# Optimization experiments

Hardware: AMD Instinct MI355X
Metric: run time of the kernel (lower is better)

## Reference

```python
import jax, jax.numpy as jnp
import numpy as np

B, N, D, H = 16, 1024, 768, 12
HD = D // H
SCALE = HD ** -0.5


def setup_inputs() -> dict:
    key = jax.random.key(0)
    ks = jax.random.split(key, 7)
    s = D ** -0.5
    return {
        "x": jax.random.normal(ks[0], (B, N, D), dtype=jnp.float32),
        "Wq": jax.random.normal(ks[1], (D, D), dtype=jnp.float32) * s,
        "bq": jax.random.normal(ks[2], (D,), dtype=jnp.float32) * 0.01,
        "Wk": jax.random.normal(ks[3], (D, D), dtype=jnp.float32) * s,
        "bk": jax.random.normal(ks[4], (D,), dtype=jnp.float32) * 0.01,
        "Wv": jax.random.normal(ks[5], (D, D), dtype=jnp.float32) * s,
        "bv": jax.random.normal(ks[6], (D,), dtype=jnp.float32) * 0.01,
    }


def _split_heads(t):
    # [B, N, D] -> [B, H, N, HD]
    return t.reshape(B, N, H, HD).transpose(0, 2, 1, 3)


def reference(x, Wq, bq, Wk, bk, Wv, bv):
    q = _split_heads(x @ Wq + bq)
    k = _split_heads(x @ Wk + bk)
    v = _split_heads(x @ Wv + bv)
    # [B, H, N, N] attention scores, fp32 softmax (matches eager path)
    scores = jnp.einsum("bhqd,bhkd->bhqk", q, k) * SCALE
    attn = jax.nn.softmax(scores.astype(jnp.float32), axis=-1).astype(q.dtype)
    # dropout p=0 in eval mode -> identity
    ctx = jnp.einsum("bhqk,bhkd->bhqd", attn, v)  # [B, H, N, HD]
    ctx = ctx.transpose(0, 2, 1, 3).reshape(B, N, D)
    return ctx
```

## Files before the change

### kernel.cpp

```cpp
#include <hip/hip_runtime.h>

#define B_ 16
#define N_ 1024
#define D_ 768
#define H_ 12
#define HD_ 64
#define QSCALE 0.18033688011112042f

typedef __attribute__((ext_vector_type(8))) __bf16 bf16x8;
typedef __attribute__((ext_vector_type(4))) float f32x4;
typedef unsigned short u16;
typedef unsigned int u32;

__device__ inline u16 f2bf(float f) {
    u32 u = __builtin_bit_cast(u32, f);
    u += 0x7fffu + ((u >> 16) & 1u);
    return (u16)(u >> 16);
}

__device__ inline float fexp2(float x) {
#if __has_builtin(__builtin_amdgcn_exp2f)
    return __builtin_amdgcn_exp2f(x);
#else
    return exp2f(x);
#endif
}

__device__ inline u32 cvt_pk_bf16(float a, float b) {
    u32 r;
    asm("v_cvt_pk_bf16_f32 %0, %1, %2" : "=v"(r) : "v"(a), "v"(b));
    return r;
}

__device__ inline void gl_lds16(const u16* gp, u16* lp_) {
    __builtin_amdgcn_global_load_lds(
        (const __attribute__((address_space(1))) u32*)(gp),
        (__attribute__((address_space(3))) u32*)(lp_), 16, 0, 0);
}

__global__ __launch_bounds__(256) void prep_kernel(
    const float* __restrict__ x, u16* __restrict__ xbf,
    const float* __restrict__ Wq, const float* __restrict__ Wk,
    const float* __restrict__ Wv, u16* __restrict__ wtall) {
    const int bid = blockIdx.x, tid = threadIdx.x;
    if (bid < 6144) {
        int i = bid * 256 + tid;
        const float4* p = (const float4*)x;
        float4 a = p[2 * i], b = p[2 * i + 1];
        union { u16 us[8]; int4 v; } u;
        u.us[0] = f2bf(a.x); u.us[1] = f2bf(a.y); u.us[2] = f2bf(a.z); u.us[3] = f2bf(a.w);
        u.us[4] = f2bf(b.x); u.us[5] = f2bf(b.y); u.us[6] = f2bf(b.z); u.us[7] = f2bf(b.w);
        ((int4*)xbf)[i] = u.v;
    } else {
        __shared__ u16 t[32][33];
        int wb = bid - 6144;
        int z = wb / 576, rem = wb % 576;
        int bx = rem % 24, by = rem / 24;
        const float* W = z == 0 ? Wq : (z == 1 ? Wk : Wv);
        u16* Wt = wtall + (size_t)z * D_ * D_;
        int n0 = bx * 32, k0 = by * 32;
        int tx = tid & 31, ty = tid >> 5;
#pragma unroll
        for (int i = 0; i < 4; i++) {
            int k = k0 + ty + i * 8;
            t[ty + i * 8][tx] = f2bf(W[k * D_ + n0 + tx]);
        }
        __syncthreads();
#pragma unroll
        for (int i = 0; i < 4; i++) {
            int n = n0 + ty + i * 8;
            Wt[n * D_ + k0 + tx] = t[tx][ty + i * 8];
        }
    }
}

__global__ __launch_bounds__(512, 2) void qkv2_kernel(
    const u16* __restrict__ xbf, const u16* __restrict__ wtall,
    const float* __restrict__ bq, const float* __restrict__ bk, const float* __restrict__ bv,
    u16* __restrict__ qbf, u16* __restrict__ kbf, u16* __restrict__ vtbf) {
    __shared__ u16 lsA[4 * 8192];
    __shared__ u16 lsB[4 * 8192];

    const int mt = blockIdx.x, nt = blockIdx.y;
    const int tid = threadIdx.x, w = tid >> 6, lane = tid & 63;
    const int g = lane >> 4, c = lane & 15;
    const int wm = w >> 2, wn = w & 3;
    const int m0 = mt * 256, n0 = nt * 192;

    const int srow = w * 16 + (lane >> 2);
    const int gch = (lane & 3) ^ ((lane >> 3) & 3);
    const u16* sa0 = xbf + (size_t)(m0 + srow) * D_ + gch * 8;
    const u16* sa1 = xbf + (size_t)(m0 + 128 + srow) * D_ + gch * 8;
    const u16* sb0 = wtall + (size_t)(n0 + srow) * D_ + gch * 8;
    const u16* sb1 = wtall + (size_t)(n0 + 128 + srow) * D_ + gch * 8;

#define STAGEP(slot, p) do {                                          \
        gl_lds16(sa0 + (p) * 32, &lsA[(slot) * 8192 + w * 512]);        \
        gl_lds16(sa1 + (p) * 32, &lsA[(slot) * 8192 + 4096 + w * 512]); \
        gl_lds16(sb0 + (p) * 32, &lsB[(slot) * 8192 + w * 512]);        \
        gl_lds16(sb1 + (p) * 32, &lsB[(slot) * 8192 + 4096 + w * 512]); \
    } while (0)

    f32x4 acc[8][3];
#pragma unroll
    for (int i = 0; i < 8; i++)
#pragma unroll
        for (int j = 0; j < 3; j++) acc[i][j] = (f32x4){0.f, 0.f, 0.f, 0.f};

    const int gp8 = (g ^ ((c >> 1) & 3)) * 8;

#define COMPUTE(s) do {                                                         \
        bf16x8 af[8], bfr[3];                                                   \
        _Pragma("unroll")                                                       \
        for (int fr = 0; fr < 8; fr++)                                          \
            af[fr] = *(const bf16x8*)&lsA[(s) * 8192 + (wm * 128 + fr * 16 + c) * 32 + gp8]; \
        _Pragma("unroll")                                                       \
        for (int fc = 0; fc < 3; fc++)                                          \
            bfr[fc] = *(const bf16x8*)&lsB[(s) * 8192 + (wn * 48 + fc * 16 + c) * 32 + gp8]; \
        _Pragma("unroll")                                                       \
        for (int fr = 0; fr < 8; fr++)                                          \
            _Pragma("unroll")                                                   \
            for (int fc = 0; fc < 3; fc++)                                      \
                acc[fr][fc] = __builtin_amdgcn_mfma_f32_16x16x32_bf16(          \
                    af[fr], bfr[fc], acc[fr][fc], 0, 0, 0);                     \
    } while (0)

    STAGEP(0, 0);
    STAGEP(1, 1);
    for (int p = 0; p < 22; ++p) {
        STAGEP((p + 2) & 3, p + 2);
        asm volatile("s_waitcnt vmcnt(8)" ::: "memory");
        __builtin_amdgcn_s_barrier();
        __builtin_amdgcn_sched_barrier(0);
        COMPUTE(p & 3);
    }
    asm volatile("s_waitcnt vmcnt(4)" ::: "memory");
    __builtin_amdgcn_s_barrier();
    __builtin_amdgcn_sched_barrier(0);
    COMPUTE(2);
    asm volatile("s_waitcnt vmcnt(0)" ::: "memory");
    __builtin_amdgcn_s_barrier();
    __builtin_amdgcn_sched_barrier(0);
    COMPUTE(3);
#undef STAGEP
#undef COMPUTE

    const int mode = nt >> 2;
    const int msub = nt & 3;
    const float* bias = mode == 0 ? bq : (mode == 1 ? bk : bv);
    float bb[3];
#pragma unroll
    for (int fc = 0; fc < 3; fc++) bb[fc] = bias[msub * 192 + wn * 48 + fc * 16 + c];

    if (mode < 2) {
        u16* outp = mode == 0 ? qbf : kbf;
        const float osc = mode == 0 ? QSCALE : 1.0f;
#pragma unroll
        for (int fc = 0; fc < 3; fc++) {
            int col = msub * 192 + wn * 48 + fc * 16 + c;
            int head = col >> 6, hd = col & 63;
#pragma unroll
            for (int fr = 0; fr < 8; fr++)
#pragma unroll
                for (int rr = 0; rr < 4; rr++) {
                    int m = m0 + wm * 128 + fr * 16 + g * 4 + rr;
                    int b = m >> 10, nn = m & 1023;
                    outp[(((size_t)b * H_ + head) * N_ + nn) * HD_ + hd] =
                        f2bf((acc[fr][fc][rr] + bb[fc]) * osc);
                }
        }
    } else {
#pragma unroll
        for (int fc = 0; fc < 3; fc++) {
            int col = msub * 192 + wn * 48 + fc * 16 + c;
            int head = col >> 6, hd = col & 63;
#pragma unroll
            for (int fr = 0; fr < 8; fr++) {
                int m = m0 + wm * 128 + fr * 16 + g * 4;
                int b = m >> 10, nn = m & 1023;
                union { u16 us[4]; int2 v; } u;
#pragma unroll
                for (int rr = 0; rr < 4; rr++) u.us[rr] = f2bf(acc[fr][fc][rr] + bb[fc]);
                *(int2*)&vtbf[(((size_t)b * H_ + head) * HD_ + hd) * N_ + nn] = u.v;
            }
        }
    }
}

__global__ __launch_bounds__(256) void attn_kernel(
    const u16* __restrict__ qbf, const u16* __restrict__ kbf,
    const u16* __restrict__ vtbf, float* __restrict__ out) {
    __shared__ u16 lk[2][64][72];
    __shared__ u16 lv[2][64][72];

    const int bh = blockIdx.x;
    const int qt = blockIdx.y;
    const int b = bh / H_, h = bh % H_;
    const int tid = threadIdx.x;
    const int w = tid >> 6, lane = tid & 63, g = lane >> 4, c = lane & 15;
    const int q0 = qt * 128;

    bf16x8 aq[2][2];
#pragma unroll
    for (int ss = 0; ss < 2; ss++) {
        const u16* qr = qbf + ((size_t)bh * N_ + q0 + w * 32 + ss * 16 + c) * HD_;
        aq[ss][0] = *(const bf16x8*)&qr[g * 8];
        aq[ss][1] = *(const bf16x8*)&qr[32 + g * 8];
    }

    const u16* kbase = kbf + (size_t)bh * N_ * HD_;
    const u16* vbase = vtbf + (size_t)bh * HD_ * N_;
    const int r0 = tid >> 3, c80 = (tid & 7) * 8;
    const int r1 = r0 + 32;

    int4 kreg0, kreg1, vreg0, vreg1;
#define LOADT(KV) do { \
        kreg0 = *(const int4*)(kbase + (size_t)((KV) + r0) * HD_ + c80); \
        kreg1 = *(const int4*)(kbase + (size_t)((KV) + r1) * HD_ + c80); \
        vreg0 = *(const int4*)(vbase + (size_t)r0 * N_ + (KV) + c80); \
        vreg1 = *(const int4*)(vbase + (size_t)r1 * N_ + (KV) + c80); \
    } while (0)
#define WRITET(bi) do { \
        *(int4*)&lk[bi][r0][c80] = kreg0; \
        *(int4*)&lk[bi][r1][c80] = kreg1; \
        *(int4*)&lv[bi][r0][c80] = vreg0; \
        *(int4*)&lv[bi][r1][c80] = vreg1; \
    } while (0)

    const f32x4 zf = (f32x4){0.f, 0.f, 0.f, 0.f};
    f32x4 o[2][4];
#pragma unroll
    for (int ss = 0; ss < 2; ss++)
#pragma unroll
        for (int i = 0; i < 4; i++) o[ss][i] = zf;
    float lr[2] = {0.f, 0.f};

    LOADT(0);
    WRITET(0);
    __syncthreads();
    int cur = 0;

    for (int kv0 = 0; kv0 < N_; kv0 += 64) {
        const bool more = (kv0 + 64) < N_;
        if (more) LOADT(kv0 + 64);

        f32x4 sc[2][4];
#pragma unroll
        for (int nf = 0; nf < 4; nf++) {
            bf16x8 ak0 = *(const bf16x8*)&lk[cur][nf * 16 + c][g * 8];
            bf16x8 ak1 = *(const bf16x8*)&lk[cur][nf * 16 + c][32 + g * 8];
            __builtin_amdgcn_s_setprio(1);
#pragma unroll
            for (int ss = 0; ss < 2; ss++) {
                sc[ss][nf] = __builtin_amdgcn_mfma_f32_16x16x32_bf16(ak0, aq[ss][0], zf, 0, 0, 0);
                sc[ss][nf] = __builtin_amdgcn_mfma_f32_16x16x32_bf16(ak1, aq[ss][1], sc[ss][nf], 0, 0, 0);
            }
            __builtin_amdgcn_s_setprio(0);
        }

        u32 pkk[2][4][2];
#pragma unroll
        for (int ss = 0; ss < 2; ss++) {
            f32x4 rsv = zf;
#pragma unroll
            for (int nf = 0; nf < 4; nf++) {
#pragma unroll
                for (int r = 0; r < 4; r++) sc[ss][nf][r] = fexp2(sc[ss][nf][r]);
                rsv += sc[ss][nf];
                pkk[ss][nf][0] = cvt_pk_bf16(sc[ss][nf][0], sc[ss][nf][1]);
                pkk[ss][nf][1] = cvt_pk_bf16(sc[ss][nf][2], sc[ss][nf][3]);
            }
            lr[ss] += (rsv[0] + rsv[1]) + (rsv[2] + rsv[3]);
        }

        bf16x8 pa[2][2];
#pragma unroll
        for (int ss = 0; ss < 2; ss++) {
            union { u32 ui[4]; bf16x8 v; } u0, u1;
            u0.ui[0] = pkk[ss][0][0]; u0.ui[1] = pkk[ss][0][1];
            u0.ui[2] = pkk[ss][1][0]; u0.ui[3] = pkk[ss][1][1];
            u1.ui[0] = pkk[ss][2][0]; u1.ui[1] = pkk[ss][2][1];
            u1.ui[2] = pkk[ss][3][0]; u1.ui[3] = pkk[ss][3][1];
            pa[ss][0] = u0.v; pa[ss][1] = u1.v;
        }

#pragma unroll
        for (int nf = 0; nf < 4; nf++) {
            union { int2 d[2]; bf16x8 v; } b0, b1;
            b0.d[0] = *(const int2*)&lv[cur][nf * 16 + c][4 * g];
            b0.d[1] = *(const int2*)&lv[cur][nf * 16 + c][16 + 4 * g];
            b1.d[0] = *(const int2*)&lv[cur][nf * 16 + c][32 + 4 * g];
            b1.d[1] = *(const int2*)&lv[cur][nf * 16 + c][48 + 4 * g];
            __builtin_amdgcn_s_setprio(1);
#pragma unroll
            for (int ss = 0; ss < 2; ss++) {
                o[ss][nf] = __builtin_amdgcn_mfma_f32_16x16x32_bf16(pa[ss][0], b0.v, o[ss][nf], 0, 0, 0);
                o[ss][nf] = __builtin_amdgcn_mfma_f32_16x16x32_bf16(pa[ss][1], b1.v, o[ss][nf], 0, 0, 0);
            }
            __builtin_amdgcn_s_setprio(0);
        }

        if (more) WRITET(cur ^ 1);
        __syncthreads();
        cur ^= 1;
    }
#undef LOADT
#undef WRITET

#pragma unroll
    for (int ss = 0; ss < 2; ss++) {
        float lf = lr[ss];
        lf += __shfl_xor(lf, 16);
        lf += __shfl_xor(lf, 32);
        float lq[4];
#pragma unroll
        for (int r = 0; r < 4; r++) lq[r] = __shfl(lf, g * 4 + r);
#pragma unroll
        for (int r = 0; r < 4; r++) {
            float inv = 1.f / lq[r];
            int n = q0 + w * 32 + ss * 16 + g * 4 + r;
#pragma unroll
            for (int nf = 0; nf < 4; nf++)
                out[((size_t)(b * N_ + n)) * D_ + h * HD_ + nf * 16 + c] = o[ss][nf][r] * inv;
        }
    }
}

extern "C" void kernel_launch(void* const* d_in, const int* in_sizes, int n_in,
                              void* d_out, int out_size, void* d_ws, size_t ws_size,
                              hipStream_t stream) {
    const float* x  = (const float*)d_in[0];
    const float* Wq = (const float*)d_in[1];
    const float* bq = (const float*)d_in[2];
    const float* Wk = (const float*)d_in[3];
    const float* bk = (const float*)d_in[4];
    const float* Wv = (const float*)d_in[5];
    const float* bv = (const float*)d_in[6];
    float* out = (float*)d_out;

    char* ws = (char*)d_ws;
    u16* xbf   = (u16*)ws;
    u16* wtall = (u16*)(ws + 25165824);
    u16* qbf   = (u16*)(ws + 28704768);
    u16* kbf   = (u16*)(ws + 53870592);
    u16* vtbf  = (u16*)(ws + 79036416);

    prep_kernel<<<7872, 256, 0, stream>>>(x, xbf, Wq, Wk, Wv, wtall);
    dim3 gg(64, 12);
    qkv2_kernel<<<gg, 512, 0, stream>>>(xbf, wtall, bq, bk, bv, qbf, kbf, vtbf);
    dim3 ga(192, 8);
    attn_kernel<<<ga, 256, 0, stream>>>(qbf, kbf, vtbf, out);
}
```

Before: 167.4 us.

## Read K and V tiles directly from global memory instead of LDS staging

```diff
diff --git a/kernel.cpp b/kernel.cpp
--- a/kernel.cpp
+++ b/kernel.cpp
@@ -190,9 +190,6 @@
 __global__ __launch_bounds__(256) void attn_kernel(
     const u16* __restrict__ qbf, const u16* __restrict__ kbf,
     const u16* __restrict__ vtbf, float* __restrict__ out) {
-    __shared__ u16 lk[2][64][72];
-    __shared__ u16 lv[2][64][72];
-
     const int bh = blockIdx.x;
     const int qt = blockIdx.y;
     const int b = bh / H_, h = bh % H_;
@@ -210,22 +207,6 @@
 
     const u16* kbase = kbf + (size_t)bh * N_ * HD_;
     const u16* vbase = vtbf + (size_t)bh * HD_ * N_;
-    const int r0 = tid >> 3, c80 = (tid & 7) * 8;
-    const int r1 = r0 + 32;
-
-    int4 kreg0, kreg1, vreg0, vreg1;
-#define LOADT(KV) do { \
-        kreg0 = *(const int4*)(kbase + (size_t)((KV) + r0) * HD_ + c80); \
-        kreg1 = *(const int4*)(kbase + (size_t)((KV) + r1) * HD_ + c80); \
-        vreg0 = *(const int4*)(vbase + (size_t)r0 * N_ + (KV) + c80); \
-        vreg1 = *(const int4*)(vbase + (size_t)r1 * N_ + (KV) + c80); \
-    } while (0)
-#define WRITET(bi) do { \
-        *(int4*)&lk[bi][r0][c80] = kreg0; \
-        *(int4*)&lk[bi][r1][c80] = kreg1; \
-        *(int4*)&lv[bi][r0][c80] = vreg0; \
-        *(int4*)&lv[bi][r1][c80] = vreg1; \
-    } while (0)
 
     const f32x4 zf = (f32x4){0.f, 0.f, 0.f, 0.f};
     f32x4 o[2][4];
@@ -235,20 +216,13 @@
         for (int i = 0; i < 4; i++) o[ss][i] = zf;
     float lr[2] = {0.f, 0.f};
 
-    LOADT(0);
-    WRITET(0);
-    __syncthreads();
-    int cur = 0;
-
     for (int kv0 = 0; kv0 < N_; kv0 += 64) {
-        const bool more = (kv0 + 64) < N_;
-        if (more) LOADT(kv0 + 64);
-
         f32x4 sc[2][4];
 #pragma unroll
         for (int nf = 0; nf < 4; nf++) {
-            bf16x8 ak0 = *(const bf16x8*)&lk[cur][nf * 16 + c][g * 8];
-            bf16x8 ak1 = *(const bf16x8*)&lk[cur][nf * 16 + c][32 + g * 8];
+            const u16* krow = kbase + (size_t)(kv0 + nf * 16 + c) * HD_;
+            bf16x8 ak0 = *(const bf16x8*)&krow[g * 8];
+            bf16x8 ak1 = *(const bf16x8*)&krow[32 + g * 8];
             __builtin_amdgcn_s_setprio(1);
 #pragma unroll
             for (int ss = 0; ss < 2; ss++) {
@@ -286,11 +260,12 @@
 
 #pragma unroll
         for (int nf = 0; nf < 4; nf++) {
+            const u16* vrow = vbase + (size_t)(nf * 16 + c) * N_ + kv0;
             union { int2 d[2]; bf16x8 v; } b0, b1;
-            b0.d[0] = *(const int2*)&lv[cur][nf * 16 + c][4 * g];
-            b0.d[1] = *(const int2*)&lv[cur][nf * 16 + c][16 + 4 * g];
-            b1.d[0] = *(const int2*)&lv[cur][nf * 16 + c][32 + 4 * g];
-            b1.d[1] = *(const int2*)&lv[cur][nf * 16 + c][48 + 4 * g];
+            b0.d[0] = *(const int2*)&vrow[4 * g];
+            b0.d[1] = *(const int2*)&vrow[16 + 4 * g];
+            b1.d[0] = *(const int2*)&vrow[32 + 4 * g];
+            b1.d[1] = *(const int2*)&vrow[48 + 4 * g];
             __builtin_amdgcn_s_setprio(1);
 #pragma unroll
             for (int ss = 0; ss < 2; ss++) {
@@ -299,13 +274,7 @@
             }
             __builtin_amdgcn_s_setprio(0);
         }
-
-        if (more) WRITET(cur ^ 1);
-        __syncthreads();
-        cur ^= 1;
-    }
-#undef LOADT
-#undef WRITET
+    }
 
 #pragma unroll
     for (int ss = 0; ss < 2; ss++) {
```

Result: slower. 389.6 us (+132.7%).
